# Kernel optimization log

Measured on AMD Instinct MI355X. Metric: run time of the kernel, lower is better.

## Reference

```python
import jax, jax.numpy as jnp
import numpy as np

# ---- Cl(4,1) geometric-product Cayley table: gp(a,b)[k] = a[i] b[j] C[i,j,k] ----
def _build_cayley():
    metric = np.array([1.0, 1.0, 1.0, 1.0, -1.0], dtype=np.float32)  # signature (4,1)
    C = np.zeros((32, 32, 32), dtype=np.float32)
    for a in range(32):
        for b in range(32):
            # canonical reordering sign (count of swaps to merge blades)
            cnt = 0
            ash = a >> 1
            while ash:
                cnt += bin(ash & b).count('1')
                ash >>= 1
            s = -1.0 if (cnt & 1) else 1.0
            common = a & b
            for i in range(5):
                if (common >> i) & 1:
                    s *= metric[i]
            C[a, b, a ^ b] = s
    return C

CAYLEY = _build_cayley()
N_HEADS = 8

def gp_cl41(a, b, C):
    # a, b: (..., 32) multivectors
    return jnp.einsum('...i,...j,ijk->...k', a, b, C)

def normalize_cl41(x, eps=1e-6):
    n = jnp.sqrt(jnp.sum(x * x, axis=-1, keepdims=True) + eps)
    return x / n

def vlinear(x, w, b):
    # x: (..., Din, 32), w: (Dout, Din), b: (Dout, 32) -- blade-wise channel mixing
    return jnp.einsum('...ik,oi->...ok', x, w) + b

def layernorm2d(x, w, b, eps=1e-5):
    # normalized_shape = [D, 32]
    m = jnp.mean(x, axis=(-2, -1), keepdims=True)
    v = jnp.var(x, axis=(-2, -1), keepdims=True)
    return (x - m) / jnp.sqrt(v + eps) * w + b

def attention(x, wq, bq, wk, bk, wv, bv, wo, bo):
    B, S, D, K = x.shape
    hd = D // N_HEADS
    q = vlinear(x, wq, bq).reshape(B, S, N_HEADS, hd, K)
    k = vlinear(x, wk, bk).reshape(B, S, N_HEADS, hd, K)
    v = vlinear(x, wv, bv).reshape(B, S, N_HEADS, hd, K)
    scores = jnp.einsum('bqhdk,bshdk->bhqs', q, k) / jnp.sqrt(jnp.float32(hd * K))
    p = jax.nn.softmax(scores, axis=-1)
    o = jnp.einsum('bhqs,bshdk->bqhdk', p, v).reshape(B, S, D, K)
    return vlinear(o, wo, bo)


def setup_inputs() -> dict:
    key = jax.random.key(0)
    B, S, D, K = 4, 512, 256, 32
    L, E, NC = 2, 4, 1000
    ks = jax.random.split(key, 24)
    s = 1.0 / np.sqrt(D)
    inp = {
        'x': jax.random.normal(ks[0], (B, S, D, K), jnp.float32),
        'ln1_w': jnp.ones((L, D, K), jnp.float32),
        'ln1_b': jnp.zeros((L, D, K), jnp.float32),
        'wq': jax.random.normal(ks[1], (L, D, D), jnp.float32) * s,
        'bq': jnp.zeros((L, D, K), jnp.float32),
        'wk': jax.random.normal(ks[2], (L, D, D), jnp.float32) * s,
        'bk': jnp.zeros((L, D, K), jnp.float32),
        'wv': jax.random.normal(ks[3], (L, D, D), jnp.float32) * s,
        'bv': jnp.zeros((L, D, K), jnp.float32),
        'wo': jax.random.normal(ks[4], (L, D, D), jnp.float32) * s,
        'bo': jnp.zeros((L, D, K), jnp.float32),
        'ln2_w': jnp.ones((L, D, K), jnp.float32),
        'ln2_b': jnp.zeros((L, D, K), jnp.float32),
        'w1': jax.random.normal(ks[5], (L, E * D, D), jnp.float32) * s,
        'b1': jnp.zeros((L, E * D, K), jnp.float32),
        'w2': jax.random.normal(ks[6], (L, D, E * D), jnp.float32) * (1.0 / np.sqrt(E * D)),
        'b2': jnp.zeros((L, D, K), jnp.float32),
        'wr': jax.random.normal(ks[7], (D, D), jnp.float32) * s,
        'br': jnp.zeros((D, K), jnp.float32),
        'wc': jax.random.normal(ks[8], (NC, D * K), jnp.float32) * 0.02,
        'bc': jnp.zeros((NC,), jnp.float32),
    }
    return inp


def reference(x, ln1_w, ln1_b, wq, bq, wk, bk, wv, bv, wo, bo,
              ln2_w, ln2_b, w1, b1, w2, b2, wr, br, wc, bc):
    C = jnp.asarray(CAYLEY)
    L = ln1_w.shape[0]
    for l in range(L):
        h = layernorm2d(x, ln1_w[l], ln1_b[l])
        x = x + attention(h, wq[l], bq[l], wk[l], bk[l], wv[l], bv[l], wo[l], bo[l])
        x = normalize_cl41(x)
        h = layernorm2d(x, ln2_w[l], ln2_b[l])
        h = jnp.tanh(vlinear(h, w1[l], b1[l]))
        x = x + vlinear(h, w2[l], b2[l])
        x = normalize_cl41(x)
    # Recursive Rotor Accumulator pooling: psi_{t+1} = normalize(gp(r_t, psi_t))
    delta = vlinear(x, wr, br)                    # (B, S, D, 32)
    B, S, D, K = delta.shape
    psi0 = jnp.zeros((B, D, K), x.dtype).at[..., 0].set(1.0)
    def step(psi, r_t):
        return normalize_cl41(gp_cl41(r_t, psi, C)), None
    psi, _ = jax.lax.scan(step, psi0, jnp.moveaxis(delta, 1, 0))
    logits = psi.reshape(B, D * K) @ wc.T + bc
    return logits
```

## Files before the change

kernel.cpp:

```cpp
#include <hip/hip_runtime.h>
#include <hip/hip_bf16.h>
#include <cstdint>
#include <cstddef>

typedef __bf16 bf16_t;
typedef __attribute__((ext_vector_type(8))) __bf16 bf16x8;
typedef __attribute__((ext_vector_type(4))) __bf16 bf16x4;
typedef __attribute__((ext_vector_type(4))) float f32x4;

#define DEV __device__ __forceinline__

DEV void async16(const bf16_t* g, bf16_t* l) {
  __builtin_amdgcn_global_load_lds((const __attribute__((address_space(1))) void*)g,
                                   (__attribute__((address_space(3))) void*)l, 16, 0, 0);
}

DEV float fast_tanh(float x) {
  const float ex = __expf(2.f * x);
  return 1.f - 2.f / (ex + 1.f);
}

enum { EPI_RESID = 0, EPI_FFN1 = 1, EPI_QKV = 2, EPI_SCORE = 3, EPI_PV = 4, EPI_DELTAT = 5 };

template<int EPI, bool TRANSB>
__global__ __launch_bounds__(256, 2)
void gemm_k(const bf16_t* __restrict__ A, const bf16_t* __restrict__ A2,
            const bf16_t* __restrict__ B, const bf16_t* __restrict__ B2,
            const float* __restrict__ bias, void* __restrict__ outp, void* __restrict__ outp2,
            int Kd, int lda, int ldb, long aStride, long bStride)
{
  __shared__ bf16_t sA[128 * 32];
  __shared__ bf16_t sB[128 * 32];
  __shared__ bf16_t sA2[128 * 32];
  __shared__ bf16_t sB2[128 * 32];

  const int tid  = threadIdx.x;
  const int lane = tid & 63;
  const int wv   = tid >> 6;
  const int wr   = wv >> 1, wc = wv & 1;

  unsigned gx = gridDim.x, gy = gridDim.y;
  unsigned nb = gx * gy * gridDim.z;
  unsigned fid = blockIdx.x + gx * (blockIdx.y + gy * blockIdx.z);
  if ((nb & 7u) == 0u) fid = (fid & 7u) * (nb >> 3) + (fid >> 3);
  const unsigned bxu = fid % gx;
  const unsigned rem = fid / gx;
  const unsigned byu = rem % gy;
  const unsigned bzu = rem / gy;
  const int m0 = byu * 128;
  const int n0 = bxu * 128;
  const int bz = bzu;

  const bf16_t *Ab, *Bb, *A2b, *B2b;
  if constexpr (EPI == EPI_SCORE) {
    const int h = bz & 7;
    const long ho = (long)(bz >> 3) * 512;
    Ab  = A  + (long)h * aStride + ho;
    Bb  = B  + (long)h * bStride + ho;
    A2b = A2 + (long)h * aStride + ho;
    B2b = B2 + (long)h * bStride + ho;
  } else {
    Ab  = A  + (long)bz * aStride;
    Bb  = B  + (long)bz * bStride;
    A2b = A2 + (long)bz * aStride;
    B2b = B2 + (long)bz * bStride;
  }

  const int sRow = tid >> 2;
  const int sKo  = (tid & 3) * 8;
  const int tr = tid & 15;
  const int tc = tid >> 4;

  f32x4 acc[4][4];
#pragma unroll
  for (int i = 0; i < 4; i++)
#pragma unroll
    for (int j = 0; j < 4; j++) acc[i][j] = f32x4{0.f, 0.f, 0.f, 0.f};

  const int ns  = Kd >> 5;
  const int off = (int)(fid & (unsigned)(ns - 1));
  for (int si = 0; si < ns; si++) {
    const int kt = ((si + off) & (ns - 1)) << 5;
    const bf16_t* ga  = Ab  + (long)(m0 + sRow) * lda + kt + sKo;
    const bf16_t* ga2 = A2b + (long)(m0 + sRow) * lda + kt + sKo;
    async16(ga,             sA  + tid * 8);
    async16(ga + 64 * lda,  sA  + 2048 + tid * 8);
    async16(ga2,            sA2 + tid * 8);
    async16(ga2 + 64 * lda, sA2 + 2048 + tid * 8);
    uint4 br0, br1, br2, br3;
    if (!TRANSB) {
      const bf16_t* gb  = Bb  + (long)(n0 + sRow) * ldb + kt + sKo;
      const bf16_t* gb2 = B2b + (long)(n0 + sRow) * ldb + kt + sKo;
      async16(gb,             sB  + tid * 8);
      async16(gb + 64 * ldb,  sB  + 2048 + tid * 8);
      async16(gb2,            sB2 + tid * 8);
      async16(gb2 + 64 * ldb, sB2 + 2048 + tid * 8);
    } else {
      const bf16_t* gb  = Bb  + (long)(kt + tr) * ldb + n0 + tc * 8;
      const bf16_t* gb2 = B2b + (long)(kt + tr) * ldb + n0 + tc * 8;
      br0 = *(const uint4*)gb;
      br1 = *(const uint4*)(gb + 16 * ldb);
      br2 = *(const uint4*)gb2;
      br3 = *(const uint4*)(gb2 + 16 * ldb);
    }
    asm volatile("s_waitcnt vmcnt(0)" ::: "memory");
    if (TRANSB) {
      const bf16_t* e0 = (const bf16_t*)&br0;
      const bf16_t* e1 = (const bf16_t*)&br1;
      const bf16_t* e2 = (const bf16_t*)&br2;
      const bf16_t* e3 = (const bf16_t*)&br3;
#pragma unroll
      for (int j = 0; j < 8; j++) {
        sB [(tc * 8 + j) * 32 + tr]      = e0[j];
        sB [(tc * 8 + j) * 32 + tr + 16] = e1[j];
        sB2[(tc * 8 + j) * 32 + tr]      = e2[j];
        sB2[(tc * 8 + j) * 32 + tr + 16] = e3[j];
      }
    }
    __syncthreads();

    bf16x8 af[4], bfr[4], af2[4], bf2[4];
#pragma unroll
    for (int i = 0; i < 4; i++) {
      const int ao = (wr * 64 + i * 16 + (lane & 15)) * 32 + (lane >> 4) * 8;
      const int bo = (wc * 64 + i * 16 + (lane & 15)) * 32 + (lane >> 4) * 8;
      af[i]  = *(const bf16x8*)&sA[ao];
      af2[i] = *(const bf16x8*)&sA2[ao];
      bfr[i] = *(const bf16x8*)&sB[bo];
      bf2[i] = *(const bf16x8*)&sB2[bo];
    }
#pragma unroll
    for (int i = 0; i < 4; i++)
#pragma unroll
      for (int j = 0; j < 4; j++) {
        acc[i][j] = __builtin_amdgcn_mfma_f32_16x16x32_bf16(af[i],  bfr[j], acc[i][j], 0, 0, 0);
        acc[i][j] = __builtin_amdgcn_mfma_f32_16x16x32_bf16(af[i],  bf2[j], acc[i][j], 0, 0, 0);
        acc[i][j] = __builtin_amdgcn_mfma_f32_16x16x32_bf16(af2[i], bfr[j], acc[i][j], 0, 0, 0);
      }
    __syncthreads();
  }

  const int cn = lane & 15;
  const int rg = (lane >> 4) * 4;
#pragma unroll
  for (int i = 0; i < 4; i++) {
    const int mb = m0 + wr * 64 + i * 16 + rg;
#pragma unroll
    for (int j = 0; j < 4; j++) {
      const int n = n0 + wc * 64 + j * 16 + cn;
#pragma unroll
      for (int r = 0; r < 4; r++) {
        const int m = mb + r;
        const float v = acc[i][j][r];
        if constexpr (EPI == EPI_RESID) {
          const float bb = bias ? bias[n * 32 + (m & 31)] : 0.f;
          ((float*)outp)[(long)m * 256 + n] += v + bb;
        } else if constexpr (EPI == EPI_QKV) {
          const int s = m >> 5, kb = m & 31;
          const int proj = n >> 8, col = n & 255;
          const int h = col >> 5, dd = col & 31;
          const long oidx = (long)proj * 4194304 + (long)(h * 512 + s) * 1024 + kb * 32 + dd;
          const float t = v + bias[n * 32 + kb];
          const bf16_t hh = (bf16_t)t;
          ((bf16_t*)outp)[oidx]  = hh;
          ((bf16_t*)outp2)[oidx] = (bf16_t)(t - (float)hh);
        } else if constexpr (EPI == EPI_SCORE) {
          const int h = bz & 7, half = bz >> 3;
          float* dst = half ? (float*)outp2 : (float*)outp;
          dst[(long)h * 262144 + (long)m * 512 + n] = v * (1.f / 32.f);
        } else if constexpr (EPI == EPI_PV) {
          const int kb = n >> 5, dd = n & 31;
          const long oidx = (long)(m * 32 + kb) * 256 + bz * 32 + dd;
          const bf16_t hh = (bf16_t)v;
          ((bf16_t*)outp)[oidx]  = hh;
          ((bf16_t*)outp2)[oidx] = (bf16_t)(v - (float)hh);
        } else {
          const int b = m >> 14, t = (m >> 5) & 511, kb = m & 31;
          ((float*)outp)[(((long)(b * 256 + n) * 512 + t) * 32) + kb] = v + bias[n * 32 + kb];
        }
      }
    }
  }
}

__global__ __launch_bounds__(512, 1)
void ffn_k(const bf16_t* __restrict__ Ah, const bf16_t* __restrict__ Al,
           const bf16_t* __restrict__ W1h_, const bf16_t* __restrict__ W1l_,
           const bf16_t* __restrict__ W2h_, const bf16_t* __restrict__ W2l_,
           const float* __restrict__ b1, const float* __restrict__ b2,
           float* __restrict__ XT)
{
  __shared__ bf16_t sAh[64 * 256], sAl[64 * 256];
  __shared__ bf16_t sWh[8192], sWl[8192];
  __shared__ bf16_t sHh[64 * 136], sHl[64 * 136];

  const int tid  = threadIdx.x;
  const int lane = tid & 63;
  const int wv   = tid >> 6;
  const int wm   = wv >> 2;
  const int wn   = wv & 3;
  const int l15  = lane & 15;
  const int lg   = lane >> 4;
  const int m0   = blockIdx.x * 64;
  const int coff = blockIdx.x & 7;
  const int soff = (blockIdx.x >> 3) & 7;
  const int toff = (blockIdx.x >> 3) & 3;

#pragma unroll
  for (int r = 0; r < 4; r++) {
    const int idx = r * 512 + tid;
    const int row = idx >> 5, cp = idx & 31;
    const int c = cp ^ (row & 31);
    async16(Ah + (long)(m0 + row) * 256 + c * 8, sAh + idx * 8);
    async16(Al + (long)(m0 + row) * 256 + c * 8, sAl + idx * 8);
  }
  asm volatile("s_waitcnt vmcnt(0)" ::: "memory");
  __syncthreads();

  f32x4 acc2[2][4];
#pragma unroll
  for (int i = 0; i < 2; i++)
#pragma unroll
    for (int j = 0; j < 4; j++) acc2[i][j] = f32x4{0.f, 0.f, 0.f, 0.f};

  const int wrow = tid >> 2;
  const int wc1  = (tid & 3) ^ (wrow & 3);

#pragma unroll 1
  for (int cc = 0; cc < 8; cc++) {
    const int ch = (cc + coff) & 7;
    const bf16_t* W1h = W1h_ + (long)(ch * 128) * 256;
    const bf16_t* W1l = W1l_ + (long)(ch * 128) * 256;
    async16(W1h + (long)wrow * 256 + soff * 32 + wc1 * 8, sWh + tid * 8);
    async16(W1l + (long)wrow * 256 + soff * 32 + wc1 * 8, sWl + tid * 8);
    asm volatile("s_waitcnt vmcnt(0)" ::: "memory");
    __syncthreads();

    f32x4 acc1[2][2];
#pragma unroll
    for (int i = 0; i < 2; i++)
#pragma unroll
      for (int j = 0; j < 2; j++) acc1[i][j] = f32x4{0.f, 0.f, 0.f, 0.f};

    for (int s = 0; s < 8; s++) {
      const int cb = (s & 1) * 4096;
      const int sp = (s + soff) & 7;
      if (s < 7) {
        const int nbuf = ((s + 1) & 1) * 4096;
        const int spn = (s + 1 + soff) & 7;
        async16(W1h + (long)wrow * 256 + spn * 32 + wc1 * 8, sWh + nbuf + tid * 8);
        async16(W1l + (long)wrow * 256 + spn * 32 + wc1 * 8, sWl + nbuf + tid * 8);
      }
      bf16x8 a_h[2], a_l[2], w_h[2], w_l[2];
#pragma unroll
      for (int i = 0; i < 2; i++) {
        const int arow = wm * 32 + i * 16 + l15;
        const int ac = (sp * 4 + lg) ^ (arow & 31);
        a_h[i] = *(const bf16x8*)&sAh[arow * 256 + ac * 8];
        a_l[i] = *(const bf16x8*)&sAl[arow * 256 + ac * 8];
      }
#pragma unroll
      for (int j = 0; j < 2; j++) {
        const int nrow = wn * 32 + j * 16 + l15;
        const int ncp = lg ^ (nrow & 3);
        w_h[j] = *(const bf16x8*)&sWh[cb + nrow * 32 + ncp * 8];
        w_l[j] = *(const bf16x8*)&sWl[cb + nrow * 32 + ncp * 8];
      }
#pragma unroll
      for (int i = 0; i < 2; i++)
#pragma unroll
        for (int j = 0; j < 2; j++) {
          acc1[i][j] = __builtin_amdgcn_mfma_f32_16x16x32_bf16(w_h[j], a_h[i], acc1[i][j], 0, 0, 0);
          acc1[i][j] = __builtin_amdgcn_mfma_f32_16x16x32_bf16(w_h[j], a_l[i], acc1[i][j], 0, 0, 0);
          acc1[i][j] = __builtin_amdgcn_mfma_f32_16x16x32_bf16(w_l[j], a_h[i], acc1[i][j], 0, 0, 0);
        }
      asm volatile("s_waitcnt vmcnt(0)" ::: "memory");
      __syncthreads();
    }

    uint4 wrg_h[2], wrg_l[2];
#pragma unroll
    for (int r = 0; r < 2; r++) {
      const int idx = r * 512 + tid;
      const int row = idx >> 2;
      const int c = (idx & 3) ^ (row & 3);
      wrg_h[r] = *(const uint4*)(W2h_ + (long)row * 1024 + ch * 128 + toff * 32 + c * 8);
      wrg_l[r] = *(const uint4*)(W2l_ + (long)row * 1024 + ch * 128 + toff * 32 + c * 8);
    }

#pragma unroll
    for (int i = 0; i < 2; i++) {
      const int m = wm * 32 + i * 16 + l15;
      const int kb = (m0 + m) & 31;
#pragma unroll
      for (int j = 0; j < 2; j++) {
        const int nb4 = wn * 32 + j * 16 + lg * 4;
        bf16x4 h4, l4;
#pragma unroll
        for (int rr = 0; rr < 4; rr++) {
          const int n = nb4 + rr;
          const float t = fast_tanh(acc1[i][j][rr] + b1[(ch * 128 + n) * 32 + kb]);
          const bf16_t hh = (bf16_t)t;
          h4[rr] = hh;
          l4[rr] = (bf16_t)(t - (float)hh);
        }
        *(bf16x4*)&sHh[m * 136 + nb4] = h4;
        *(bf16x4*)&sHl[m * 136 + nb4] = l4;
      }
    }
    __syncthreads();

    for (int t = 0; t < 4; t++) {
      const int tp = (t + toff) & 3;
#pragma unroll
      for (int r = 0; r < 2; r++) {
        const int idx = r * 512 + tid;
        *(uint4*)&sWh[idx * 8] = wrg_h[r];
        *(uint4*)&sWl[idx * 8] = wrg_l[r];
      }
      __syncthreads();
      if (t < 3) {
        const int tpn = (t + 1 + toff) & 3;
#pragma unroll
        for (int r = 0; r < 2; r++) {
          const int idx = r * 512 + tid;
          const int row = idx >> 2;
          const int c = (idx & 3) ^ (row & 3);
          wrg_h[r] = *(const uint4*)(W2h_ + (long)row * 1024 + ch * 128 + tpn * 32 + c * 8);
          wrg_l[r] = *(const uint4*)(W2l_ + (long)row * 1024 + ch * 128 + tpn * 32 + c * 8);
        }
      }
      bf16x8 h_h[2], h_l[2], v_h[4], v_l[4];
#pragma unroll
      for (int i = 0; i < 2; i++) {
        const int hrow = wm * 32 + i * 16 + l15;
        h_h[i] = *(const bf16x8*)&sHh[hrow * 136 + tp * 32 + lg * 8];
        h_l[i] = *(const bf16x8*)&sHl[hrow * 136 + tp * 32 + lg * 8];
      }
#pragma unroll
      for (int j = 0; j < 4; j++) {
        const int n2 = wn * 64 + j * 16 + l15;
        const int ncp = lg ^ (n2 & 3);
        v_h[j] = *(const bf16x8*)&sWh[n2 * 32 + ncp * 8];
        v_l[j] = *(const bf16x8*)&sWl[n2 * 32 + ncp * 8];
      }
#pragma unroll
      for (int i = 0; i < 2; i++)
#pragma unroll
        for (int j = 0; j < 4; j++) {
          acc2[i][j] = __builtin_amdgcn_mfma_f32_16x16x32_bf16(h_h[i], v_h[j], acc2[i][j], 0, 0, 0);
          acc2[i][j] = __builtin_amdgcn_mfma_f32_16x16x32_bf16(h_h[i], v_l[j], acc2[i][j], 0, 0, 0);
          acc2[i][j] = __builtin_amdgcn_mfma_f32_16x16x32_bf16(h_l[i], v_h[j], acc2[i][j], 0, 0, 0);
        }
      __syncthreads();
    }
  }

#pragma unroll
  for (int i = 0; i < 2; i++)
#pragma unroll
    for (int j = 0; j < 4; j++) {
      const int n2 = wn * 64 + j * 16 + l15;
#pragma unroll
      for (int rr = 0; rr < 4; rr++) {
        const int m = m0 + wm * 32 + i * 16 + lg * 4 + rr;
        XT[(long)m * 256 + n2] += acc2[i][j][rr] + b2[n2 * 32 + (m & 31)];
      }
    }
}

__global__ __launch_bounds__(256)
void transpose_k(const float* __restrict__ src, float* __restrict__ dst, int R, int C)
{
  __shared__ float t[32][33];
  const long boff = (long)blockIdx.z * R * C;
  const int r0 = blockIdx.y * 32, c0 = blockIdx.x * 32;
  const int tx = threadIdx.x & 31, ty = threadIdx.x >> 5;
#pragma unroll
  for (int i = 0; i < 32; i += 8)
    t[ty + i][tx] = src[boff + (long)(r0 + ty + i) * C + c0 + tx];
  __syncthreads();
#pragma unroll
  for (int i = 0; i < 32; i += 8)
    dst[boff + (long)(c0 + ty + i) * R + r0 + tx] = t[tx][ty + i];
}

DEV void hilo4(const f32x4 t, bf16x4& h, bf16x4& l) {
#pragma unroll
  for (int j = 0; j < 4; j++) {
    const bf16_t hh = (bf16_t)t[j];
    h[j] = hh;
    l[j] = (bf16_t)(t[j] - (float)hh);
  }
}

template<int MODE>
__global__ __launch_bounds__(256)
void nl_k(const float* __restrict__ X, float* __restrict__ Xo,
          const float* __restrict__ wT, const float* __restrict__ bT,
          bf16_t* __restrict__ oh, bf16_t* __restrict__ ol)
{
  const int row = blockIdx.x * 4 + (threadIdx.x >> 6);
  const int l   = threadIdx.x & 63;
  const float4* Xr = (const float4*)X + (long)row * 2048 + l;
  f32x4 v[32];
#pragma unroll
  for (int kb = 0; kb < 32; kb++) {
    const float4 t = Xr[kb * 64];
    v[kb] = f32x4{t.x, t.y, t.z, t.w};
  }
  if constexpr (MODE & 1) {
    f32x4 ss = f32x4{1e-6f, 1e-6f, 1e-6f, 1e-6f};
#pragma unroll
    for (int kb = 0; kb < 32; kb++) ss += v[kb] * v[kb];
    const f32x4 rs = f32x4{rsqrtf(ss[0]), rsqrtf(ss[1]), rsqrtf(ss[2]), rsqrtf(ss[3])};
#pragma unroll
    for (int kb = 0; kb < 32; kb++) v[kb] *= rs;
    if constexpr (MODE & 2) {
      float4* Xw = (float4*)Xo + (long)row * 2048 + l;
#pragma unroll
      for (int kb = 0; kb < 32; kb++)
        Xw[kb * 64] = float4{v[kb][0], v[kb][1], v[kb][2], v[kb][3]};
    }
  }
  if constexpr (MODE & 4) {
    float s = 0.f, s2 = 0.f;
#pragma unroll
    for (int kb = 0; kb < 32; kb++) {
      s  += (v[kb][0] + v[kb][1]) + (v[kb][2] + v[kb][3]);
      s2 += (v[kb][0] * v[kb][0] + v[kb][1] * v[kb][1]) +
            (v[kb][2] * v[kb][2] + v[kb][3] * v[kb][3]);
    }
#pragma unroll
    for (int o = 32; o > 0; o >>= 1) { s += __shfl_xor(s, o); s2 += __shfl_xor(s2, o); }
    const float mean = s * (1.f / 8192.f);
    const float var  = s2 * (1.f / 8192.f) - mean * mean;
    const float rstd = rsqrtf(var + 1e-5f);
    const float4* w4 = (const float4*)wT + l;
    const float4* b4 = (const float4*)bT + l;
#pragma unroll
    for (int kb = 0; kb < 32; kb++) {
      const float4 ww = w4[kb * 64];
      const float4 bb = b4[kb * 64];
      f32x4 t;
      t[0] = (v[kb][0] - mean) * rstd * ww.x + bb.x;
      t[1] = (v[kb][1] - mean) * rstd * ww.y + bb.y;
      t[2] = (v[kb][2] - mean) * rstd * ww.z + bb.z;
      t[3] = (v[kb][3] - mean) * rstd * ww.w + bb.w;
      bf16x4 h4, l4;
      hilo4(t, h4, l4);
      const long oi = (long)row * 8192 + kb * 256 + l * 4;
      *(bf16x4*)&oh[oi] = h4;
      *(bf16x4*)&ol[oi] = l4;
    }
  }
  if constexpr (MODE & 8) {
#pragma unroll
    for (int kb = 0; kb < 32; kb++) {
      bf16x4 h4, l4;
      hilo4(v[kb], h4, l4);
      const long oi = (long)row * 8192 + kb * 256 + l * 4;
      *(bf16x4*)&oh[oi] = h4;
      *(bf16x4*)&ol[oi] = l4;
    }
  }
}

__global__ __launch_bounds__(256)
void softmax_k(const float* __restrict__ SC, const float* __restrict__ SC2,
               bf16_t* __restrict__ Ph, bf16_t* __restrict__ Pl)
{
  const int row = blockIdx.x * 4 + (threadIdx.x >> 6);
  const int lane = threadIdx.x & 63;
  const float* s1 = SC  + (long)row * 512;
  const float* s2 = SC2 + (long)row * 512;
  float4 a = *(const float4*)&s1[lane * 4];
  float4 c = *(const float4*)&s1[256 + lane * 4];
  const float4 a2 = *(const float4*)&s2[lane * 4];
  const float4 c2 = *(const float4*)&s2[256 + lane * 4];
  a.x += a2.x; a.y += a2.y; a.z += a2.z; a.w += a2.w;
  c.x += c2.x; c.y += c2.y; c.z += c2.z; c.w += c2.w;
  float mx = fmaxf(fmaxf(fmaxf(a.x, a.y), fmaxf(a.z, a.w)),
                   fmaxf(fmaxf(c.x, c.y), fmaxf(c.z, c.w)));
#pragma unroll
  for (int o = 32; o > 0; o >>= 1) mx = fmaxf(mx, __shfl_xor(mx, o));
  float e[8] = {expf(a.x - mx), expf(a.y - mx), expf(a.z - mx), expf(a.w - mx),
                expf(c.x - mx), expf(c.y - mx), expf(c.z - mx), expf(c.w - mx)};
  float sum = ((e[0] + e[1]) + (e[2] + e[3])) + ((e[4] + e[5]) + (e[6] + e[7]));
#pragma unroll
  for (int o = 32; o > 0; o >>= 1) sum += __shfl_xor(sum, o);
  const float inv = 1.f / sum;
  bf16x4 h0, h1, l0, l1;
#pragma unroll
  for (int j = 0; j < 4; j++) {
    const float p0 = e[j] * inv, p1 = e[4 + j] * inv;
    h0[j] = (bf16_t)p0; l0[j] = (bf16_t)(p0 - (float)h0[j]);
    h1[j] = (bf16_t)p1; l1[j] = (bf16_t)(p1 - (float)h1[j]);
  }
  *(bf16x4*)&Ph[(long)row * 512 + lane * 4] = h0;
  *(bf16x4*)&Ph[(long)row * 512 + 256 + lane * 4] = h1;
  *(bf16x4*)&Pl[(long)row * 512 + lane * 4] = l0;
  *(bf16x4*)&Pl[(long)row * 512 + 256 + lane * 4] = l1;
}

constexpr float gpsign(int i, int j) {
  int cnt = 0;
  for (int s = 1; s < 5; s++) cnt += __builtin_popcount((i >> s) & j);
  float sgn = (cnt & 1) ? -1.f : 1.f;
  if ((i & j) & 16) sgn = -sgn;
  return sgn;
}

DEV void gp32(const float* __restrict__ a, const float* __restrict__ b, float* __restrict__ o) {
#pragma unroll
  for (int k = 0; k < 32; k++) {
    float s0 = 0.f, s1 = 0.f;
#pragma unroll
    for (int i = 0; i < 32; i += 2) {
      s0 = fmaf(gpsign(i, i ^ k) * a[i], b[i ^ k], s0);
      s1 = fmaf(gpsign(i + 1, (i + 1) ^ k) * a[i + 1], b[(i + 1) ^ k], s1);
    }
    o[k] = s0 + s1;
  }
}

__global__ __launch_bounds__(256)
void gptree_k(const float* __restrict__ dT, float* __restrict__ psiO)
{
  __shared__ float bufA[256 * 33];
  __shared__ float bufB[128 * 33];
  const int chain = blockIdx.x;
  const int t = threadIdx.x;
  const float* src = dT + (long)chain * (512 * 32);
  {
    float v[64];
    const float4* g = (const float4*)(src + t * 64);
#pragma unroll
    for (int i = 0; i < 16; i++) *(float4*)&v[i * 4] = g[i];
    float o[32];
    gp32(v + 32, v, o);
    float ss = 1e-6f;
#pragma unroll
    for (int k = 0; k < 32; k++) ss = fmaf(o[k], o[k], ss);
    const float rs = rsqrtf(ss);
#pragma unroll
    for (int k = 0; k < 32; k++) bufA[t * 33 + k] = o[k] * rs;
  }
  __syncthreads();
  int cur = 0;
#pragma unroll 1
  for (int P = 128; P >= 1; P >>= 1) {
    const float* in = cur ? bufB : bufA;
    float* ob = cur ? bufA : bufB;
    if (t < P) {
      float a[32], b[32], o[32];
#pragma unroll
      for (int c = 0; c < 32; c++) { b[c] = in[t * 66 + c]; a[c] = in[t * 66 + 33 + c]; }
      gp32(a, b, o);
      float ss = 1e-6f;
#pragma unroll
      for (int k = 0; k < 32; k++) ss = fmaf(o[k], o[k], ss);
      const float rs = rsqrtf(ss);
#pragma unroll
      for (int k = 0; k < 32; k++) ob[t * 33 + k] = o[k] * rs;
    }
    cur ^= 1;
    __syncthreads();
  }
  if (t < 32) psiO[(long)chain * 32 + t] = (cur ? bufB : bufA)[t];
}

__global__ __launch_bounds__(256)
void cls_k(const float* __restrict__ psi, const float* __restrict__ wcw,
           const float* __restrict__ bc, float* __restrict__ out)
{
  const int c = blockIdx.x;
  const int tid = threadIdx.x;
  float a0 = 0.f, a1 = 0.f, a2 = 0.f, a3 = 0.f;
  for (int i = tid * 4; i < 8192; i += 1024) {
    const float4 w  = *(const float4*)&wcw[(long)c * 8192 + i];
    const float4 p0 = *(const float4*)&psi[i];
    const float4 p1 = *(const float4*)&psi[8192 + i];
    const float4 p2 = *(const float4*)&psi[16384 + i];
    const float4 p3 = *(const float4*)&psi[24576 + i];
    a0 += w.x * p0.x + w.y * p0.y + w.z * p0.z + w.w * p0.w;
    a1 += w.x * p1.x + w.y * p1.y + w.z * p1.z + w.w * p1.w;
    a2 += w.x * p2.x + w.y * p2.y + w.z * p2.z + w.w * p2.w;
    a3 += w.x * p3.x + w.y * p3.y + w.z * p3.z + w.w * p3.w;
  }
#pragma unroll
  for (int o = 32; o > 0; o >>= 1) {
    a0 += __shfl_down(a0, o); a1 += __shfl_down(a1, o);
    a2 += __shfl_down(a2, o); a3 += __shfl_down(a3, o);
  }
  __shared__ float red[4][4];
  const int wv = tid >> 6;
  if ((tid & 63) == 0) { red[wv][0] = a0; red[wv][1] = a1; red[wv][2] = a2; red[wv][3] = a3; }
  __syncthreads();
  if (tid < 4) {
    const float r = red[0][tid] + red[1][tid] + red[2][tid] + red[3][tid] + bc[c];
    out[(long)tid * 1000 + c] = r;
  }
}

__global__ void split_k(const float* __restrict__ in, bf16_t* __restrict__ h,
                        bf16_t* __restrict__ l, int n)
{
  const int i = blockIdx.x * 256 + threadIdx.x;
  if (i < n) {
    const float v = in[i];
    const bf16_t hh = (bf16_t)v;
    h[i] = hh;
    l[i] = (bf16_t)(v - (float)hh);
  }
}

__global__ void cpy_k(const float* __restrict__ in, float* __restrict__ o, int n)
{
  const int i = blockIdx.x * 256 + threadIdx.x;
  if (i < n) o[i] = in[i];
}

extern "C" void kernel_launch(void* const* d_in, const int* in_sizes, int n_in,
                              void* d_out, int out_size, void* d_ws, size_t ws_size,
                              hipStream_t stream)
{
  const float* x    = (const float*)d_in[0];
  const float* ln1w = (const float*)d_in[1];
  const float* ln1b = (const float*)d_in[2];
  const float* wq   = (const float*)d_in[3];
  const float* bq   = (const float*)d_in[4];
  const float* wk   = (const float*)d_in[5];
  const float* bk   = (const float*)d_in[6];
  const float* wvv  = (const float*)d_in[7];
  const float* bv   = (const float*)d_in[8];
  const float* wo   = (const float*)d_in[9];
  const float* bo   = (const float*)d_in[10];
  const float* ln2w = (const float*)d_in[11];
  const float* ln2b = (const float*)d_in[12];
  const float* w1   = (const float*)d_in[13];
  const float* b1   = (const float*)d_in[14];
  const float* w2   = (const float*)d_in[15];
  const float* b2   = (const float*)d_in[16];
  const float* wr   = (const float*)d_in[17];
  const float* br   = (const float*)d_in[18];
  const float* wcw  = (const float*)d_in[19];
  const float* bc   = (const float*)d_in[20];
  float* out = (float*)d_out;

  char* ws = (char*)d_ws;
  const size_t MB = 1ull << 20;
  const size_t KB = 1024;
  float*  XT   = (float*)(ws + 0);
  bf16_t* HBh  = (bf16_t*)(ws + 64 * MB);
  bf16_t* HBl  = (bf16_t*)(ws + 96 * MB);
  bf16_t* QKVh = (bf16_t*)(ws + 128 * MB);
  bf16_t* QKVl = (bf16_t*)(ws + 152 * MB);
  float*  SCb  = (float*)(ws + 176 * MB);
  float*  SC2b = (float*)(ws + 184 * MB);
  bf16_t* Ph   = QKVh;
  bf16_t* Pl   = QKVl;
  bf16_t* OBh  = QKVh + 4194304;
  bf16_t* OBl  = QKVl + 4194304;
  bf16_t* Vh   = QKVh + 8388608;
  bf16_t* Vl   = QKVl + 8388608;
  bf16_t* XHI = (bf16_t*)(ws + 64 * MB), *XLO = (bf16_t*)(ws + 96 * MB);
  float*  DELTAT = (float*)(ws + 128 * MB);
  float*  PSI  = (float*)(ws + 192 * MB);
  char*   W    = ws + 193 * MB;
  bf16_t* WQKVh = (bf16_t*)(W);
  bf16_t* WQKVl = (bf16_t*)(W + 1 * MB);
  bf16_t* W1h = (bf16_t*)(W + 2 * MB);   bf16_t* W1l = (bf16_t*)(W + 3 * MB);
  bf16_t* W2h = (bf16_t*)(W + 4 * MB);   bf16_t* W2l = (bf16_t*)(W + 5 * MB);
  bf16_t* WOh = (bf16_t*)(W + 6 * MB);   bf16_t* WOl = (bf16_t*)(W + 6 * MB + 256 * KB);
  bf16_t* WRh = (bf16_t*)(W + 6 * MB + 512 * KB);
  bf16_t* WRl = (bf16_t*)(W + 6 * MB + 640 * KB);
  float*  BQKV = (float*)(W + 6 * MB + 768 * KB);
  float*  LNT  = (float*)(W + 6 * MB + 960 * KB);
  float* LN1WT = LNT, *LN1BT = LNT + 16384, *LN2WT = LNT + 32768, *LN2BT = LNT + 49152;

  for (int l = 0; l < 2; l++) {
    split_k<<<256, 256, 0, stream>>>(wq + l * 65536, WQKVh + l * 196608, WQKVl + l * 196608, 65536);
    split_k<<<256, 256, 0, stream>>>(wk + l * 65536, WQKVh + l * 196608 + 65536, WQKVl + l * 196608 + 65536, 65536);
    split_k<<<256, 256, 0, stream>>>(wvv + l * 65536, WQKVh + l * 196608 + 131072, WQKVl + l * 196608 + 131072, 65536);
    cpy_k<<<32, 256, 0, stream>>>(bq + l * 8192, BQKV + l * 24576, 8192);
    cpy_k<<<32, 256, 0, stream>>>(bk + l * 8192, BQKV + l * 24576 + 8192, 8192);
    cpy_k<<<32, 256, 0, stream>>>(bv + l * 8192, BQKV + l * 24576 + 16384, 8192);
  }
  split_k<<<512, 256, 0, stream>>>(wo, WOh, WOl, 131072);
  split_k<<<2048, 256, 0, stream>>>(w1, W1h, W1l, 524288);
  split_k<<<2048, 256, 0, stream>>>(w2, W2h, W2l, 524288);
  split_k<<<256, 256, 0, stream>>>(wr, WRh, WRl, 65536);
  transpose_k<<<dim3(1, 8, 2), 256, 0, stream>>>(ln1w, LN1WT, 256, 32);
  transpose_k<<<dim3(1, 8, 2), 256, 0, stream>>>(ln1b, LN1BT, 256, 32);
  transpose_k<<<dim3(1, 8, 2), 256, 0, stream>>>(ln2w, LN2WT, 256, 32);
  transpose_k<<<dim3(1, 8, 2), 256, 0, stream>>>(ln2b, LN2BT, 256, 32);

  transpose_k<<<dim3(1, 8, 2048), 256, 0, stream>>>(x, XT, 256, 32);

  for (int l = 0; l < 2; l++) {
    if (l == 0)
      nl_k<4><<<512, 256, 0, stream>>>(XT, nullptr, LN1WT, LN1BT, HBh, HBl);
    for (int b = 0; b < 4; b++) {
      const long ao = (long)b * 16384 * 256;
      gemm_k<EPI_QKV, false><<<dim3(6, 128, 1), 256, 0, stream>>>(
          HBh + ao, HBl + ao, WQKVh + l * 196608, WQKVl + l * 196608,
          BQKV + l * 24576, QKVh, QKVl, 256, 256, 256, 0, 0);
      gemm_k<EPI_SCORE, false><<<dim3(4, 4, 16), 256, 0, stream>>>(
          QKVh, QKVl, QKVh + 4194304, QKVl + 4194304,
          nullptr, SCb, SC2b, 512, 1024, 1024, 512 * 1024, 512 * 1024);
      softmax_k<<<1024, 256, 0, stream>>>(SCb, SC2b, Ph, Pl);
      gemm_k<EPI_PV, true><<<dim3(8, 4, 8), 256, 0, stream>>>(
          Ph, Pl, Vh, Vl, nullptr, OBh, OBl, 512, 512, 1024, 512 * 512, 512 * 1024);
      gemm_k<EPI_RESID, false><<<dim3(2, 128, 1), 256, 0, stream>>>(
          OBh, OBl, WOh + l * 65536, WOl + l * 65536,
          bo + l * 8192, (float*)XT + ao, nullptr, 256, 256, 256, 0, 0);
    }
    nl_k<1 | 2 | 4><<<512, 256, 0, stream>>>(XT, XT, LN2WT + l * 8192, LN2BT + l * 8192, HBh, HBl);
    ffn_k<<<1024, 512, 0, stream>>>(HBh, HBl,
                                    W1h + l * 262144, W1l + l * 262144,
                                    W2h + l * 262144, W2l + l * 262144,
                                    b1 + l * 32768, b2 + l * 8192, XT);
    if (l == 0) {
      nl_k<1 | 2 | 4><<<512, 256, 0, stream>>>(XT, XT, LN1WT + 8192, LN1BT + 8192, HBh, HBl);
    } else {
      nl_k<1 | 8><<<512, 256, 0, stream>>>(XT, nullptr, nullptr, nullptr, XHI, XLO);
    }
  }

  gemm_k<EPI_DELTAT, false><<<dim3(2, 512, 1), 256, 0, stream>>>(
      XHI, XLO, WRh, WRl, br, DELTAT, nullptr, 256, 256, 256, 0, 0);
  gptree_k<<<1024, 256, 0, stream>>>(DELTAT, PSI);
  cls_k<<<1000, 256, 0, stream>>>(PSI, wcw, bc, out);
}
```

Measured before the change: 2.215 ms.

## Double-buffer GEMM shared tiles and prefetch FFN weights through registers

The generic GEMM kernel now keeps two shared-memory stages, issuing loads for the next K-slice before computing the current one and waiting with a partial vmcnt, so global latency overlaps the MFMA work. The fused FFN kernel switches W1 staging from async LDS loads to register prefetch two steps ahead, stored into the alternate buffer, which removes the per-step full vmcnt wait. The b1 bias values are hoisted into registers before the chunk. Shared memory in the GEMM doubles to 64KB, which may cut occupancy below the launch bound of 2 blocks, and register pressure rises.

```diff
diff --git a/kernel.cpp b/kernel.cpp
--- a/kernel.cpp
+++ b/kernel.cpp
@@ -29,10 +29,10 @@
             const float* __restrict__ bias, void* __restrict__ outp, void* __restrict__ outp2,
             int Kd, int lda, int ldb, long aStride, long bStride)
 {
-  __shared__ bf16_t sA[128 * 32];
-  __shared__ bf16_t sB[128 * 32];
-  __shared__ bf16_t sA2[128 * 32];
-  __shared__ bf16_t sB2[128 * 32];
+  __shared__ bf16_t sA [2][4096];
+  __shared__ bf16_t sB [2][4096];
+  __shared__ bf16_t sA2[2][4096];
+  __shared__ bf16_t sB2[2][4096];
 
   const int tid  = threadIdx.x;
   const int lane = tid & 63;
@@ -79,42 +79,63 @@
 
   const int ns  = Kd >> 5;
   const int off = (int)(fid & (unsigned)(ns - 1));
-  for (int si = 0; si < ns; si++) {
+
+  uint4 br0, br1, br2, br3;
+
+  auto stageA = [&](int si, int b) {
     const int kt = ((si + off) & (ns - 1)) << 5;
     const bf16_t* ga  = Ab  + (long)(m0 + sRow) * lda + kt + sKo;
     const bf16_t* ga2 = A2b + (long)(m0 + sRow) * lda + kt + sKo;
-    async16(ga,             sA  + tid * 8);
-    async16(ga + 64 * lda,  sA  + 2048 + tid * 8);
-    async16(ga2,            sA2 + tid * 8);
-    async16(ga2 + 64 * lda, sA2 + 2048 + tid * 8);
-    uint4 br0, br1, br2, br3;
-    if (!TRANSB) {
-      const bf16_t* gb  = Bb  + (long)(n0 + sRow) * ldb + kt + sKo;
-      const bf16_t* gb2 = B2b + (long)(n0 + sRow) * ldb + kt + sKo;
-      async16(gb,             sB  + tid * 8);
-      async16(gb + 64 * ldb,  sB  + 2048 + tid * 8);
-      async16(gb2,            sB2 + tid * 8);
-      async16(gb2 + 64 * ldb, sB2 + 2048 + tid * 8);
-    } else {
-      const bf16_t* gb  = Bb  + (long)(kt + tr) * ldb + n0 + tc * 8;
-      const bf16_t* gb2 = B2b + (long)(kt + tr) * ldb + n0 + tc * 8;
-      br0 = *(const uint4*)gb;
-      br1 = *(const uint4*)(gb + 16 * ldb);
-      br2 = *(const uint4*)gb2;
-      br3 = *(const uint4*)(gb2 + 16 * ldb);
-    }
-    asm volatile("s_waitcnt vmcnt(0)" ::: "memory");
-    if (TRANSB) {
+    async16(ga,             &sA [b][tid * 8]);
+    async16(ga + 64 * lda,  &sA [b][2048 + tid * 8]);
+    async16(ga2,            &sA2[b][tid * 8]);
+    async16(ga2 + 64 * lda, &sA2[b][2048 + tid * 8]);
+  };
+  auto stageB = [&](int si, int b) {
+    const int kt = ((si + off) & (ns - 1)) << 5;
+    const bf16_t* gb  = Bb  + (long)(n0 + sRow) * ldb + kt + sKo;
+    const bf16_t* gb2 = B2b + (long)(n0 + sRow) * ldb + kt + sKo;
+    async16(gb,             &sB [b][tid * 8]);
+    async16(gb + 64 * ldb,  &sB [b][2048 + tid * 8]);
+    async16(gb2,            &sB2[b][tid * 8]);
+    async16(gb2 + 64 * ldb, &sB2[b][2048 + tid * 8]);
+  };
+  auto loadBR = [&](int si) {
+    const int kt = ((si + off) & (ns - 1)) << 5;
+    const bf16_t* gb  = Bb  + (long)(kt + tr) * ldb + n0 + tc * 8;
+    const bf16_t* gb2 = B2b + (long)(kt + tr) * ldb + n0 + tc * 8;
+    br0 = *(const uint4*)gb;
+    br1 = *(const uint4*)(gb + 16 * ldb);
+    br2 = *(const uint4*)gb2;
+    br3 = *(const uint4*)(gb2 + 16 * ldb);
+  };
+
+  stageA(0, 0);
+  if constexpr (!TRANSB) stageB(0, 0); else loadBR(0);
+
+  for (int si = 0; si < ns; si++) {
+    const int cb = si & 1;
+    if (si + 1 < ns) stageA(si + 1, cb ^ 1);
+    if constexpr (TRANSB) {
       const bf16_t* e0 = (const bf16_t*)&br0;
       const bf16_t* e1 = (const bf16_t*)&br1;
       const bf16_t* e2 = (const bf16_t*)&br2;
       const bf16_t* e3 = (const bf16_t*)&br3;
 #pragma unroll
       for (int j = 0; j < 8; j++) {
-        sB [(tc * 8 + j) * 32 + tr]      = e0[j];
-        sB [(tc * 8 + j) * 32 + tr + 16] = e1[j];
-        sB2[(tc * 8 + j) * 32 + tr]      = e2[j];
-        sB2[(tc * 8 + j) * 32 + tr + 16] = e3[j];
+        sB [cb][(tc * 8 + j) * 32 + tr]      = e0[j];
+        sB [cb][(tc * 8 + j) * 32 + tr + 16] = e1[j];
+        sB2[cb][(tc * 8 + j) * 32 + tr]      = e2[j];
+        sB2[cb][(tc * 8 + j) * 32 + tr + 16] = e3[j];
+      }
+      if (si + 1 < ns) loadBR(si + 1);
+      if (si + 1 >= ns) asm volatile("s_waitcnt vmcnt(0)" ::: "memory");
+    } else {
+      if (si + 1 < ns) {
+        stageB(si + 1, cb ^ 1);
+        asm volatile("s_waitcnt vmcnt(8)" ::: "memory");
+      } else {
+        asm volatile("s_waitcnt vmcnt(0)" ::: "memory");
       }
     }
     __syncthreads();
@@ -124,10 +145,10 @@
     for (int i = 0; i < 4; i++) {
       const int ao = (wr * 64 + i * 16 + (lane & 15)) * 32 + (lane >> 4) * 8;
       const int bo = (wc * 64 + i * 16 + (lane & 15)) * 32 + (lane >> 4) * 8;
-      af[i]  = *(const bf16x8*)&sA[ao];
-      af2[i] = *(const bf16x8*)&sA2[ao];
-      bfr[i] = *(const bf16x8*)&sB[bo];
-      bf2[i] = *(const bf16x8*)&sB2[bo];
+      af[i]  = *(const bf16x8*)&sA [cb][ao];
+      af2[i] = *(const bf16x8*)&sA2[cb][ao];
+      bfr[i] = *(const bf16x8*)&sB [cb][bo];
+      bf2[i] = *(const bf16x8*)&sB2[cb][bo];
     }
 #pragma unroll
     for (int i = 0; i < 4; i++)
@@ -224,16 +245,37 @@
     for (int j = 0; j < 4; j++) acc2[i][j] = f32x4{0.f, 0.f, 0.f, 0.f};
 
   const int wrow = tid >> 2;
-  const int wc1  = (tid & 3) ^ (wrow & 3);
+  const int tc4  = tid & 3;
+  const int wls  = wrow * 32 + ((tc4 ^ (wrow & 3)) * 8);
 
 #pragma unroll 1
   for (int cc = 0; cc < 8; cc++) {
     const int ch = (cc + coff) & 7;
     const bf16_t* W1h = W1h_ + (long)(ch * 128) * 256;
     const bf16_t* W1l = W1l_ + (long)(ch * 128) * 256;
-    async16(W1h + (long)wrow * 256 + soff * 32 + wc1 * 8, sWh + tid * 8);
-    async16(W1l + (long)wrow * 256 + soff * 32 + wc1 * 8, sWl + tid * 8);
-    asm volatile("s_waitcnt vmcnt(0)" ::: "memory");
+
+    float b1v[2][2][4];
+#pragma unroll
+    for (int i = 0; i < 2; i++) {
+      const int kb = (wm * 32 + i * 16 + l15) & 31;
+#pragma unroll
+      for (int j = 0; j < 2; j++)
+#pragma unroll
+        for (int rr = 0; rr < 4; rr++)
+          b1v[i][j][rr] = b1[(ch * 128 + wn * 32 + j * 16 + lg * 4 + rr) * 32 + kb];
+    }
+
+    uint4 rh[2], rl[2];
+    {
+      const int sp0 = soff & 7;
+      const int sp1 = (1 + soff) & 7;
+      rh[0] = *(const uint4*)(W1h + (long)wrow * 256 + sp0 * 32 + tc4 * 8);
+      rl[0] = *(const uint4*)(W1l + (long)wrow * 256 + sp0 * 32 + tc4 * 8);
+      rh[1] = *(const uint4*)(W1h + (long)wrow * 256 + sp1 * 32 + tc4 * 8);
+      rl[1] = *(const uint4*)(W1l + (long)wrow * 256 + sp1 * 32 + tc4 * 8);
+    }
+    *(uint4*)&sWh[wls] = rh[0];
+    *(uint4*)&sWl[wls] = rl[0];
     __syncthreads();
 
     f32x4 acc1[2][2];
@@ -242,15 +284,20 @@
 #pragma unroll
       for (int j = 0; j < 2; j++) acc1[i][j] = f32x4{0.f, 0.f, 0.f, 0.f};
 
+#pragma unroll
     for (int s = 0; s < 8; s++) {
       const int cb = (s & 1) * 4096;
+      if (s < 7) {
+        const int nb = ((s + 1) & 1) * 4096;
+        *(uint4*)&sWh[nb + wls] = rh[(s + 1) & 1];
+        *(uint4*)&sWl[nb + wls] = rl[(s + 1) & 1];
+      }
+      if (s < 6) {
+        const int spn = (s + 2 + soff) & 7;
+        rh[s & 1] = *(const uint4*)(W1h + (long)wrow * 256 + spn * 32 + tc4 * 8);
+        rl[s & 1] = *(const uint4*)(W1l + (long)wrow * 256 + spn * 32 + tc4 * 8);
+      }
       const int sp = (s + soff) & 7;
-      if (s < 7) {
-        const int nbuf = ((s + 1) & 1) * 4096;
-        const int spn = (s + 1 + soff) & 7;
-        async16(W1h + (long)wrow * 256 + spn * 32 + wc1 * 8, sWh + nbuf + tid * 8);
-        async16(W1l + (long)wrow * 256 + spn * 32 + wc1 * 8, sWl + nbuf + tid * 8);
-      }
       bf16x8 a_h[2], a_l[2], w_h[2], w_l[2];
 #pragma unroll
       for (int i = 0; i < 2; i++) {
@@ -274,7 +321,6 @@
           acc1[i][j] = __builtin_amdgcn_mfma_f32_16x16x32_bf16(w_h[j], a_l[i], acc1[i][j], 0, 0, 0);
           acc1[i][j] = __builtin_amdgcn_mfma_f32_16x16x32_bf16(w_l[j], a_h[i], acc1[i][j], 0, 0, 0);
         }
-      asm volatile("s_waitcnt vmcnt(0)" ::: "memory");
       __syncthreads();
     }
 
@@ -291,15 +337,13 @@
 #pragma unroll
     for (int i = 0; i < 2; i++) {
       const int m = wm * 32 + i * 16 + l15;
-      const int kb = (m0 + m) & 31;
 #pragma unroll
       for (int j = 0; j < 2; j++) {
         const int nb4 = wn * 32 + j * 16 + lg * 4;
         bf16x4 h4, l4;
 #pragma unroll
         for (int rr = 0; rr < 4; rr++) {
-          const int n = nb4 + rr;
-          const float t = fast_tanh(acc1[i][j][rr] + b1[(ch * 128 + n) * 32 + kb]);
+          const float t = fast_tanh(acc1[i][j][rr] + b1v[i][j][rr]);
           const bf16_t hh = (bf16_t)t;
           h4[rr] = hh;
           l4[rr] = (bf16_t)(t - (float)hh);
```

New measurement: 2.470 ms. 11.5% more time.
